# Optimization experiments

Measured on AMD Instinct MI355X. Metric: run time of the kernel, lower is better.

Reference implementation:

```python
import jax, jax.numpy as jnp
import numpy as np

TEMP = 0.3  # softmax temperature used in load-balance loss


def setup_inputs() -> dict:
    key = jax.random.key(0)
    k1, k2 = jax.random.split(key)
    num_tokens, d_model, num_expert = 16384, 4096, 128
    inp = jax.random.normal(k1, (num_tokens, d_model), dtype=jnp.float32)
    wg = jax.random.normal(k2, (num_expert, d_model), dtype=jnp.float32) * (1.0 / np.sqrt(d_model))
    return {"inp": inp, "wg": wg, "top_k": 2}


def reference(inp, wg, top_k):
    # Gate logits: [T, E] = [T, D] @ [D, E]
    logits = jnp.einsum("td,ed->te", inp, wg)
    # Top-k selection + softmax over the k selected logits
    top_vals, top_idx = jax.lax.top_k(logits, top_k)  # [T, k]
    gate_score = jax.nn.softmax(top_vals, axis=-1)    # [T, k]
    # Load-balance loss (stored as self.loss in torch; returned here)
    T, E = logits.shape
    probs = jax.nn.softmax(logits / TEMP, axis=-1)    # [T, E]
    mask = jax.nn.one_hot(top_idx[:, 0], E, dtype=probs.dtype) * (E / T)
    me = jnp.sum(probs, axis=0)                       # [E]
    ce = jnp.sum(mask, axis=0)                        # [E]
    loss = jnp.sum(me * ce) / T
    return top_idx, gate_score, loss
```

## Files before the change

### kernel.cpp

```cpp
#include <hip/hip_runtime.h>

typedef _Float16 half8 __attribute__((ext_vector_type(8)));
typedef float floatx4 __attribute__((ext_vector_type(4)));

#define NTOK 16384
#define DM   4096
#define NE   128
#define MT   32
#define BK   64
#define NITER (DM / BK)
#define NBLK (NTOK / MT)
#define TEMP 0.3f
#define CSTRIDE 528
#define ABUF (8 * CSTRIDE)
#define BUFSZ (2 * ABUF)

__global__ void pack_b_kernel(const float* __restrict__ wg, _Float16* __restrict__ Bp) {
    int gtid = blockIdx.x * blockDim.x + threadIdx.x;
    int l  = gtid & 63;
    int tg = gtid >> 6;
    int g  = tg & 7;
    int kc = tg >> 3;
    const float* src = wg + (size_t)(g * 16 + (l & 15)) * DM + kc * 32 + (l >> 4) * 8;
    float4 v0 = *(const float4*)src;
    float4 v1 = *(const float4*)(src + 4);
    float f[8] = {v0.x, v0.y, v0.z, v0.w, v1.x, v1.y, v1.z, v1.w};
    half8 h1, h2;
#pragma unroll
    for (int j = 0; j < 8; j++) {
        h1[j] = (_Float16)f[j];
        h2[j] = (_Float16)((f[j] - (float)h1[j]) * 2048.0f);
    }
    char* dst = (char*)Bp + (size_t)tg * 2048 + l * 16;
    *(half8*)dst = h1;
    *(half8*)(dst + 1024) = h2;
}

__device__ __forceinline__ void stage_write(unsigned char* base, unsigned off,
                                            float4 v0, float4 v1) {
    float f[8] = {v0.x, v0.y, v0.z, v0.w, v1.x, v1.y, v1.z, v1.w};
    half8 h1, h2;
#pragma unroll
    for (int j = 0; j < 8; j++) {
        h1[j] = (_Float16)f[j];
        h2[j] = (_Float16)((f[j] - (float)h1[j]) * 2048.0f);
    }
    *(half8*)(base + off) = h1;
    *(half8*)(base + ABUF + off) = h2;
}

__launch_bounds__(256, 2)
__global__ void moe_gate_kernel(const float* __restrict__ A,
                                const _Float16* __restrict__ Bp,
                                float* __restrict__ out,
                                float* __restrict__ me_part,
                                float* __restrict__ ce_part) {
    __shared__ __align__(16) unsigned char smem[17664];
    const int tid  = threadIdx.x;
    const int wave = tid >> 6;
    const int lane = tid & 63;
    const int quad = lane >> 4;
    const int lrow = lane & 15;
    const int tok0 = blockIdx.x * MT;

    const int srow = tid >> 3;
    const int schunk = tid & 7;
    const float* aptr = A + (size_t)(tok0 + srow) * DM + schunk * 8;
    const unsigned swoff = schunk * CSTRIDE + srow * 16;

    const unsigned aroff = quad * CSTRIDE + lrow * 16;

    const char* bB = (const char*)Bp + (wave * 2) * 2048 + lane * 16;

    floatx4 accm[2][2], accc[2][2];
#pragma unroll
    for (int r = 0; r < 2; r++)
#pragma unroll
        for (int c = 0; c < 2; c++) {
            accm[r][c] = (floatx4){0.f, 0.f, 0.f, 0.f};
            accc[r][c] = (floatx4){0.f, 0.f, 0.f, 0.f};
        }

    {
        float4 v0 = *(const float4*)aptr;
        float4 v1 = *(const float4*)(aptr + 4);
        stage_write(smem, swoff, v0, v1);
    }
    __syncthreads();

    for (int it = 0; it < NITER; ++it) {
        float4 n0, n1;
        if (it < NITER - 1) {
            const float* p = aptr + (it + 1) * BK;
            n0 = *(const float4*)p;
            n1 = *(const float4*)(p + 4);
        }
        unsigned char* cb = smem + (it & 1) * BUFSZ;
        const char* bit = bB + (size_t)it * 32768;

#pragma unroll
        for (int ks = 0; ks < 2; ++ks) {
            half8 b1f[2], b2f[2], a1[2], a2[2];
#pragma unroll
            for (int c = 0; c < 2; c++) {
                b1f[c] = *(const half8*)(bit + ks * 16384 + c * 2048);
                b2f[c] = *(const half8*)(bit + ks * 16384 + c * 2048 + 1024);
            }
#pragma unroll
            for (int r = 0; r < 2; r++) {
                a1[r] = *(const half8*)(cb + ks * 2112 + r * 256 + aroff);
                a2[r] = *(const half8*)(cb + ABUF + ks * 2112 + r * 256 + aroff);
            }
#pragma unroll
            for (int r = 0; r < 2; r++)
#pragma unroll
                for (int c = 0; c < 2; c++) {
                    accm[r][c] = __builtin_amdgcn_mfma_f32_16x16x32_f16(a1[r], b1f[c], accm[r][c], 0, 0, 0);
                    accc[r][c] = __builtin_amdgcn_mfma_f32_16x16x32_f16(a1[r], b2f[c], accc[r][c], 0, 0, 0);
                    accc[r][c] = __builtin_amdgcn_mfma_f32_16x16x32_f16(a2[r], b1f[c], accc[r][c], 0, 0, 0);
                }
        }
        if (it < NITER - 1)
            stage_write(smem + ((it + 1) & 1) * BUFSZ, swoff, n0, n1);
        __syncthreads();
    }

    float* LG     = (float*)smem;
    float* tmax   = (float*)(smem + 16896);
    float* tscale = tmax + 32;
    int*   hist   = (int*)(tscale + 32);

#pragma unroll
    for (int r = 0; r < 2; r++)
#pragma unroll
        for (int c = 0; c < 2; c++) {
            int e = wave * 32 + c * 16 + lrow;
#pragma unroll
            for (int g = 0; g < 4; g++) {
                int t = r * 16 + quad * 4 + g;
                LG[e * 33 + t] = accm[r][c][g] + accc[r][c][g] * (1.0f / 2048.0f);
            }
        }
    if (tid < NE) hist[tid] = 0;
    __syncthreads();

    if (tid < MT) {
        const int t = tid;
        float m1 = -1e30f, m2 = -1e30f;
        int i1 = 0, i2 = 0;
        for (int e = 0; e < NE; e++) {
            float v = LG[e * 33 + t];
            if (v > m1) { m2 = m1; i2 = i1; m1 = v; i1 = e; }
            else if (v > m2) { m2 = v; i2 = e; }
        }
        float s = 0.f;
        for (int e = 0; e < NE; e++)
            s += __expf((LG[e * 33 + t] - m1) * (1.0f / TEMP));
        tmax[t] = m1;
        tscale[t] = 1.0f / s;
        atomicAdd(&hist[i1], 1);

        const int tg = tok0 + t;
        out[tg * 2 + 0] = (float)i1;
        out[tg * 2 + 1] = (float)i2;
        float d = __expf(m2 - m1);
        float g1 = 1.0f / (1.0f + d);
        out[2 * NTOK + tg * 2 + 0] = g1;
        out[2 * NTOK + tg * 2 + 1] = d * g1;
    }
    __syncthreads();

    if (tid < NE) {
        const int e = tid;
        float s = 0.f;
        for (int t = 0; t < MT; t++)
            s += __expf((LG[e * 33 + t] - tmax[t]) * (1.0f / TEMP)) * tscale[t];
        me_part[blockIdx.x * NE + e] = s;
        ce_part[blockIdx.x * NE + e] = (float)hist[e];
    }
}

__global__ void finalize_kernel(const float* __restrict__ mp, const float* __restrict__ cp,
                                float* __restrict__ out) {
    __shared__ float red[2 * 8 * 128];
    __shared__ float wsum[2];
    const int tid = threadIdx.x;
    const int e = tid & 127, seg = tid >> 7;
    float sm = 0.f, sc = 0.f;
    for (int b = seg; b < NBLK; b += 8) {
        sm += mp[b * NE + e];
        sc += cp[b * NE + e];
    }
    red[seg * 128 + e] = sm;
    red[1024 + seg * 128 + e] = sc;
    __syncthreads();
    if (tid < 128) {
        float me = 0.f, ce = 0.f;
#pragma unroll
        for (int s = 0; s < 8; s++) {
            me += red[s * 128 + tid];
            ce += red[1024 + s * 128 + tid];
        }
        ce *= (float)NE / (float)NTOK;
        float v = me * ce;
#pragma unroll
        for (int off = 32; off; off >>= 1) v += __shfl_down(v, off);
        if ((tid & 63) == 0) wsum[tid >> 6] = v;
    }
    __syncthreads();
    if (tid == 0) out[4 * NTOK] = (wsum[0] + wsum[1]) / (float)NTOK;
}

extern "C" void kernel_launch(void* const* d_in, const int* in_sizes, int n_in,
                              void* d_out, int out_size, void* d_ws, size_t ws_size,
                              hipStream_t stream) {
    (void)in_sizes; (void)n_in; (void)out_size; (void)ws_size;
    const float* inp = (const float*)d_in[0];
    const float* wg  = (const float*)d_in[1];
    float* out = (float*)d_out;

    _Float16* Bp = (_Float16*)d_ws;
    float* mp = (float*)((char*)d_ws + (2u << 20));
    float* cp = mp + NBLK * NE;

    pack_b_kernel<<<256, 256, 0, stream>>>(wg, Bp);
    moe_gate_kernel<<<NBLK, 256, 0, stream>>>(inp, Bp, out, mp, cp);
    finalize_kernel<<<1, 1024, 0, stream>>>(mp, cp, out);
}
```

Measured before the change: 463.5 us.

## Split GEMM over K halves and move top-k epilogue to separate kernel

The gating GEMM is split into two K halves, doubling the block count so more blocks run concurrently, and launch bounds are raised to 4 blocks per SM. Partial logits go to a global workspace laid out expert-major. A new top-k kernel sums the two partials and computes the top-2, gate scores and load-balance partial sums over 64-token tiles. This aims to raise occupancy and shorten the tail of the memory-bound GEMM, at the cost of writing and re-reading 16 MB of partial logits plus an extra kernel launch.

```diff
diff --git a/kernel.cpp b/kernel.cpp
--- a/kernel.cpp
+++ b/kernel.cpp
@@ -8,8 +8,12 @@
 #define NE   128
 #define MT   32
 #define BK   64
-#define NITER (DM / BK)
-#define NBLK (NTOK / MT)
+#define KSPLIT 2
+#define KHALF (DM / KSPLIT)
+#define NITER (KHALF / BK)
+#define NBLK_MAIN (NTOK / MT * KSPLIT)
+#define ET   64
+#define NBLK_EPI (NTOK / ET)
 #define TEMP 0.3f
 #define CSTRIDE 528
 #define ABUF (8 * CSTRIDE)
@@ -49,28 +53,26 @@
     *(half8*)(base + ABUF + off) = h2;
 }
 
-__launch_bounds__(256, 2)
-__global__ void moe_gate_kernel(const float* __restrict__ A,
+__launch_bounds__(256, 4)
+__global__ void moe_gemm_kernel(const float* __restrict__ A,
                                 const _Float16* __restrict__ Bp,
-                                float* __restrict__ out,
-                                float* __restrict__ me_part,
-                                float* __restrict__ ce_part) {
-    __shared__ __align__(16) unsigned char smem[17664];
+                                float* __restrict__ part) {
+    __shared__ __align__(16) unsigned char smem[2 * BUFSZ];
     const int tid  = threadIdx.x;
     const int wave = tid >> 6;
     const int lane = tid & 63;
     const int quad = lane >> 4;
     const int lrow = lane & 15;
-    const int tok0 = blockIdx.x * MT;
+    const int half = blockIdx.x & 1;
+    const int tok0 = (blockIdx.x >> 1) * MT;
 
     const int srow = tid >> 3;
     const int schunk = tid & 7;
-    const float* aptr = A + (size_t)(tok0 + srow) * DM + schunk * 8;
+    const float* aptr = A + (size_t)(tok0 + srow) * DM + half * KHALF + schunk * 8;
     const unsigned swoff = schunk * CSTRIDE + srow * 16;
-
     const unsigned aroff = quad * CSTRIDE + lrow * 16;
 
-    const char* bB = (const char*)Bp + (wave * 2) * 2048 + lane * 16;
+    const char* bB = (const char*)Bp + (size_t)half * (1u << 20) + (wave * 2) * 2048 + lane * 16;
 
     floatx4 accm[2][2], accc[2][2];
 #pragma unroll
@@ -125,42 +127,70 @@
         __syncthreads();
     }
 
-    float* LG     = (float*)smem;
-    float* tmax   = (float*)(smem + 16896);
-    float* tscale = tmax + 32;
-    int*   hist   = (int*)(tscale + 32);
-
+    float* pbase = part + (size_t)half * NTOK * NE;
 #pragma unroll
     for (int r = 0; r < 2; r++)
 #pragma unroll
         for (int c = 0; c < 2; c++) {
+            floatx4 v;
+#pragma unroll
+            for (int g = 0; g < 4; g++)
+                v[g] = accm[r][c][g] + accc[r][c][g] * (1.0f / 2048.0f);
             int e = wave * 32 + c * 16 + lrow;
-#pragma unroll
-            for (int g = 0; g < 4; g++) {
-                int t = r * 16 + quad * 4 + g;
-                LG[e * 33 + t] = accm[r][c][g] + accc[r][c][g] * (1.0f / 2048.0f);
+            int t = tok0 + r * 16 + quad * 4;
+            *(floatx4*)(pbase + (size_t)e * NTOK + t) = v;
+        }
+}
+
+__global__ void topk_kernel(const float* __restrict__ part,
+                            float* __restrict__ out,
+                            float* __restrict__ me_part,
+                            float* __restrict__ ce_part) {
+    __shared__ float LG[NE * 68];
+    __shared__ float tmax[ET], tscale[ET];
+    __shared__ int hist[NE];
+    const int tid = threadIdx.x;
+    const int t0  = blockIdx.x * ET;
+    const float* p0 = part;
+    const float* p1 = part + (size_t)NTOK * NE;
+
+    {
+        const int q = tid & 3;
+#pragma unroll
+        for (int pass = 0; pass < 2; pass++) {
+            int e = (tid >> 2) + pass * 64;
+            const float* r0 = p0 + (size_t)e * NTOK + t0 + q * 16;
+            const float* r1 = p1 + (size_t)e * NTOK + t0 + q * 16;
+            float* dst = LG + e * 68 + q * 16;
+#pragma unroll
+            for (int j = 0; j < 16; j += 4) {
+                float4 a = *(const float4*)(r0 + j);
+                float4 b = *(const float4*)(r1 + j);
+                float4 s = {a.x + b.x, a.y + b.y, a.z + b.z, a.w + b.w};
+                *(float4*)(dst + j) = s;
             }
         }
+    }
     if (tid < NE) hist[tid] = 0;
     __syncthreads();
 
-    if (tid < MT) {
+    if (tid < ET) {
         const int t = tid;
         float m1 = -1e30f, m2 = -1e30f;
         int i1 = 0, i2 = 0;
         for (int e = 0; e < NE; e++) {
-            float v = LG[e * 33 + t];
+            float v = LG[e * 68 + t];
             if (v > m1) { m2 = m1; i2 = i1; m1 = v; i1 = e; }
             else if (v > m2) { m2 = v; i2 = e; }
         }
         float s = 0.f;
         for (int e = 0; e < NE; e++)
-            s += __expf((LG[e * 33 + t] - m1) * (1.0f / TEMP));
+            s += __expf((LG[e * 68 + t] - m1) * (1.0f / TEMP));
         tmax[t] = m1;
         tscale[t] = 1.0f / s;
         atomicAdd(&hist[i1], 1);
 
-        const int tg = tok0 + t;
+        const int tg = t0 + t;
         out[tg * 2 + 0] = (float)i1;
         out[tg * 2 + 1] = (float)i2;
         float d = __expf(m2 - m1);
@@ -173,8 +203,8 @@
     if (tid < NE) {
         const int e = tid;
         float s = 0.f;
-        for (int t = 0; t < MT; t++)
-            s += __expf((LG[e * 33 + t] - tmax[t]) * (1.0f / TEMP)) * tscale[t];
+        for (int t = 0; t < ET; t++)
+            s += __expf((LG[e * 68 + t] - tmax[t]) * (1.0f / TEMP)) * tscale[t];
         me_part[blockIdx.x * NE + e] = s;
         ce_part[blockIdx.x * NE + e] = (float)hist[e];
     }
@@ -187,7 +217,7 @@
     const int tid = threadIdx.x;
     const int e = tid & 127, seg = tid >> 7;
     float sm = 0.f, sc = 0.f;
-    for (int b = seg; b < NBLK; b += 8) {
+    for (int b = seg; b < NBLK_EPI; b += 8) {
         sm += mp[b * NE + e];
         sc += cp[b * NE + e];
     }
@@ -220,10 +250,12 @@
     float* out = (float*)d_out;
 
     _Float16* Bp = (_Float16*)d_ws;
-    float* mp = (float*)((char*)d_ws + (2u << 20));
-    float* cp = mp + NBLK * NE;
+    float* part = (float*)((char*)d_ws + (2u << 20));
+    float* mp = (float*)((char*)d_ws + (18u << 20));
+    float* cp = mp + NBLK_EPI * NE;
 
     pack_b_kernel<<<256, 256, 0, stream>>>(wg, Bp);
-    moe_gate_kernel<<<NBLK, 256, 0, stream>>>(inp, Bp, out, mp, cp);
+    moe_gemm_kernel<<<NBLK_MAIN, 256, 0, stream>>>(inp, Bp, part);
+    topk_kernel<<<NBLK_EPI, 256, 0, stream>>>(part, out, mp, cp);
     finalize_kernel<<<1, 1024, 0, stream>>>(mp, cp, out);
 }
```

New measurement: 426.8 us. -7.9%, faster.
